# Kernel tuning notes

Hardware: AMD Instinct MI355X
Metric: run time of the kernel (lower is better)

Reference implementation:

```python
import jax, jax.numpy as jnp
import numpy as np

H = 128
B, N, E = 256, 81, 1620
LN_EPS = 1e-5


def setup_inputs() -> dict:
    key = jax.random.key(0)
    ks = jax.random.split(key, 12)
    s = 0.05
    return {
        "node_features": jax.random.normal(ks[0], (B, N, H), jnp.float32),
        "edge_index": jax.random.randint(ks[1], (2, E), 0, N, jnp.int64),
        "Wm1": jax.random.normal(ks[2], (2 * H, H), jnp.float32) * s,
        "bm1": jnp.zeros((H,), jnp.float32),
        "Wm2": jax.random.normal(ks[3], (H, H), jnp.float32) * s,
        "bm2": jnp.zeros((H,), jnp.float32),
        "Wu1": jax.random.normal(ks[4], (2 * H, H), jnp.float32) * s,
        "bu1": jnp.zeros((H,), jnp.float32),
        "Wu2": jax.random.normal(ks[5], (H, H), jnp.float32) * s,
        "bu2": jnp.zeros((H,), jnp.float32),
        "gamma": jnp.ones((H,), jnp.float32),
        "beta": jnp.zeros((H,), jnp.float32),
    }


def reference(node_features, edge_index, Wm1, bm1, Wm2, bm2, Wu1, bu1, Wu2, bu2, gamma, beta):
    src_idx, tgt_idx = edge_index[0], edge_index[1]
    # Gather: [B, E, H] each (vectorized over batch; original loops in Python)
    src = node_features[:, src_idx]
    tgt = node_features[:, tgt_idx]
    comb = jnp.concatenate([src, tgt], axis=-1)            # [B, E, 2H]
    msgs = jax.nn.relu(comb @ Wm1 + bm1) @ Wm2 + bm2       # [B, E, H]
    # Scatter-mean aggregation at target nodes
    agg = jnp.zeros_like(node_features).at[:, tgt_idx].add(msgs)  # [B, N, H]
    counts = jnp.zeros((N,), node_features.dtype).at[tgt_idx].add(1.0)
    counts = jnp.maximum(counts, 1.0)
    agg = agg / counts[None, :, None]
    # Node update MLP + residual + LayerNorm
    comb2 = jnp.concatenate([node_features, agg], axis=-1)  # [B, N, 2H]
    upd = jax.nn.relu(comb2 @ Wu1 + bu1) @ Wu2 + bu2
    x = node_features + upd
    mu = jnp.mean(x, axis=-1, keepdims=True)
    var = jnp.mean(jnp.square(x - mu), axis=-1, keepdims=True)
    return (x - mu) * jax.lax.rsqrt(var + LN_EPS) * gamma + beta
```

## Files before the change

kernel.cpp:

```cpp
#include <hip/hip_runtime.h>


#define NN 81
#define HH 128
#define EE 1620
#define NCH 12
#define CHSZ 135
#define MPAD 96
#define WB_BYTES 196608
#define OFFS_OFF (WB_BYTES)
#define CSR_OFF  (OFFS_OFF + 82 * 4)
#define BC_OFF   (CSR_OFF + EE * 4)
#define WS_NEED  (BC_OFF + HH * 4)

typedef __attribute__((ext_vector_type(8))) short bf16x8;
typedef __attribute__((ext_vector_type(8))) unsigned short ushort8v;
typedef __attribute__((ext_vector_type(4))) unsigned short ushort4v;
typedef __attribute__((ext_vector_type(4))) float f32x4;

__device__ __forceinline__ unsigned short f2b(float f) {
  union { float f; unsigned u; } v; v.f = f;
  unsigned r = v.u + 0x7fffu + ((v.u >> 16) & 1u);
  return (unsigned short)(r >> 16);
}
__device__ __forceinline__ float b2f(unsigned short h) {
  union { unsigned u; float f; } v; v.u = ((unsigned)h) << 16;
  return v.f;
}
__device__ __forceinline__ unsigned swzu(int r, int laneb) {
  return ((unsigned)(r * 256 + laneb)) ^ ((unsigned)((r & 7) << 4));
}

__global__ __launch_bounds__(1024)
void setup_kernel(const float* __restrict__ Wm1, const float* __restrict__ Wm2,
                  const float* __restrict__ Wu1, const float* __restrict__ Wu2,
                  const float* __restrict__ bm2, const int* __restrict__ eidx,
                  char* __restrict__ ws) {
  __shared__ __align__(16) char arena[81920];
  const int tid = threadIdx.x;

  if (blockIdx.x < 8) {
    const int gid = blockIdx.x * 1024 + tid;
    const int lane = gid & 63;
    const int t = gid >> 6;
    const int ks = t & 3, nt = (t >> 2) & 7, mat = t >> 5;
    const float* src;
    int slot;
    if (mat == 0)      { src = Wm1;           slot = 0; }
    else if (mat == 1) { src = Wm1 + HH * HH; slot = 1; }
    else if (mat == 2) { src = Wu1;           slot = 3; }
    else               { src = Wu2;           slot = 5; }
    const int c = nt * 16 + (lane & 15);
    const int k0 = ks * 32 + (lane >> 4) * 8;
    bf16x8 pv;
#pragma unroll
    for (int j = 0; j < 8; ++j) pv[j] = (short)f2b(src[(k0 + j) * HH + c]);
    *(bf16x8*)((unsigned short*)ws + (size_t)slot * 16384 + (((nt * 4 + ks) * 64) + lane) * 8) = pv;
    return;
  }

  if (blockIdx.x == 8) {
    int* edg   = (int*)arena;
    int* cnt   = edg + 2 * EE;
    int* tot   = cnt + NCH * NN;
    int* scanS = tot + NN;
    int* wsumS = scanS + 128;
    int* offsS = wsumS + 2;
    int* csrS  = offsS + NN + 1;
    for (int i = tid; i < 2 * EE; i += 1024) edg[i] = eidx[i];
    __syncthreads();
    if (tid < NCH * NN) {
      const int t = tid % NN, ch = tid / NN;
      const int e0 = ch * CHSZ, e1 = e0 + CHSZ;
      int c = 0;
      for (int e = e0; e < e1; ++e) c += (edg[EE + e] == t);
      cnt[ch * NN + t] = c;
    }
    __syncthreads();
    if (tid < NN) {
      int s = 0;
#pragma unroll
      for (int ch = 0; ch < NCH; ++ch) s += cnt[ch * NN + tid];
      tot[tid] = s;
    }
    __syncthreads();
    if (tid < 128) {
      const int l = tid & 63, w = tid >> 6;
      int inc = (tid < NN) ? tot[tid] : 0;
#pragma unroll
      for (int d = 1; d < 64; d <<= 1) {
        int u = __shfl_up(inc, d);
        if (l >= d) inc += u;
      }
      scanS[tid] = inc;
      if (l == 63) wsumS[w] = inc;
    }
    __syncthreads();
    if (tid < 128) {
      const int w = tid >> 6;
      const int inc = scanS[tid] + (w ? wsumS[0] : 0);
      if (tid < NN) offsS[tid] = inc - tot[tid];
      if (tid == NN - 1) offsS[NN] = inc;
    }
    __syncthreads();
    if (tid < NCH * NN) {
      const int t = tid % NN, ch = tid / NN;
      int pos = offsS[t];
      for (int c2 = 0; c2 < ch; ++c2) pos += cnt[c2 * NN + t];
      const int e0 = ch * CHSZ, e1 = e0 + CHSZ;
      for (int e = e0; e < e1; ++e)
        if (edg[EE + e] == t) csrS[pos++] = edg[e];
    }
    __syncthreads();
    int* wofs = (int*)(ws + OFFS_OFF);
    int* wcsr = (int*)(ws + CSR_OFF);
    for (int i = tid; i < NN + 1; i += 1024) wofs[i] = offsS[i];
    for (int i = tid; i < EE; i += 1024) wcsr[i] = csrS[i];
    return;
  }

  {
    const int bs = blockIdx.x - 9;
    float* WuL = (float*)arena;
    float* WmL = WuL + HH * HH;
    const float* Wu1b = Wu1 + HH * HH;
    float4* WuL4 = (float4*)WuL;
    const float4* src4 = (const float4*)Wu1b;
    for (int i = tid; i < HH * HH / 4; i += 1024) WuL4[i] = src4[i];
    const float4* wm4 = (const float4*)(Wm2 + bs * 32 * HH);
    float4* WmL4 = (float4*)WmL;
    if (tid < 32 * HH / 4) WmL4[tid] = wm4[tid];
    __syncthreads();
    const int kk = tid >> 5;
    const int k  = bs * 32 + kk;
    const int cg = tid & 31;
    f32x4 acc = (f32x4)0.f;
    for (int j = 0; j < HH; ++j) {
      const float a = WmL[kk * HH + j];
      const float4 w = WuL4[j * 32 + cg];
      acc[0] += a * w.x; acc[1] += a * w.y; acc[2] += a * w.z; acc[3] += a * w.w;
    }
    unsigned short* dst = (unsigned short*)ws;
#pragma unroll
    for (int q = 0; q < 4; ++q) {
      const int c = cg * 4 + q;
      const int nt = c >> 4;
      const int l = (((k & 31) >> 3) << 4) | (c & 15);
      dst[(size_t)2 * 16384 + (((nt * 4 + bs) * 64) + l) * 8 + (k & 7)] = f2b(acc[q]);
    }
    if (bs == 0 && tid < HH) {
      float s = 0.f;
      for (int j = 0; j < HH; ++j) s += bm2[j] * WuL[j * HH + tid];
      ((float*)(ws + BC_OFF))[tid] = s;
    }
  }
}

__device__ __forceinline__ void gemm3x1(const unsigned short* Ab, const unsigned short* Wp,
                                        int lane, int mt0, int nt0, f32x4 acc[3]) {
  bf16x8 Bf[4];
#pragma unroll
  for (int ks = 0; ks < 4; ++ks)
    Bf[ks] = *(const bf16x8*)(Wp + ((nt0 * 4 + ks) * 64 + lane) * 8);
  const int rl = lane & 15;
  const int kb = (lane >> 4) * 16;
  const unsigned swz = (unsigned)((rl & 7) << 4);
#pragma unroll
  for (int ks = 0; ks < 4; ++ks)
#pragma unroll
    for (int mm = 0; mm < 3; ++mm) {
      const int r = (mt0 + mm) * 16 + rl;
      const unsigned byte = (unsigned)(r * 256) + (((unsigned)(ks * 64 + kb)) ^ swz);
      bf16x8 a = *(const bf16x8*)((const char*)Ab + byte);
      acc[mm] = __builtin_amdgcn_mfma_f32_16x16x32_bf16(a, Bf[ks], acc[mm], 0, 0, 0);
    }
}

__device__ __forceinline__ void gemm3x1x2(const unsigned short* Ab,
                                          const unsigned short* Wp0, const unsigned short* Wp1,
                                          int lane, int mt0, int nt0,
                                          f32x4 acc0[3], f32x4 acc1[3]) {
  bf16x8 B0[4], B1[4];
#pragma unroll
  for (int ks = 0; ks < 4; ++ks) {
    B0[ks] = *(const bf16x8*)(Wp0 + ((nt0 * 4 + ks) * 64 + lane) * 8);
    B1[ks] = *(const bf16x8*)(Wp1 + ((nt0 * 4 + ks) * 64 + lane) * 8);
  }
  const int rl = lane & 15;
  const int kb = (lane >> 4) * 16;
  const unsigned swz = (unsigned)((rl & 7) << 4);
#pragma unroll
  for (int ks = 0; ks < 4; ++ks)
#pragma unroll
    for (int mm = 0; mm < 3; ++mm) {
      const int r = (mt0 + mm) * 16 + rl;
      const unsigned byte = (unsigned)(r * 256) + (((unsigned)(ks * 64 + kb)) ^ swz);
      bf16x8 a = *(const bf16x8*)((const char*)Ab + byte);
      acc0[mm] = __builtin_amdgcn_mfma_f32_16x16x32_bf16(a, B0[ks], acc0[mm], 0, 0, 0);
      acc1[mm] = __builtin_amdgcn_mfma_f32_16x16x32_bf16(a, B1[ks], acc1[mm], 0, 0, 0);
    }
}

__device__ __forceinline__ void gemm3x1_2A(const unsigned short* A0, const unsigned short* A1,
                                           const unsigned short* Wp0, const unsigned short* Wp1,
                                           int lane, int mt0, int nt0,
                                           f32x4 acc0[3], f32x4 acc1[3]) {
  bf16x8 B0[4], B1[4];
#pragma unroll
  for (int ks = 0; ks < 4; ++ks) {
    B0[ks] = *(const bf16x8*)(Wp0 + ((nt0 * 4 + ks) * 64 + lane) * 8);
    B1[ks] = *(const bf16x8*)(Wp1 + ((nt0 * 4 + ks) * 64 + lane) * 8);
  }
  const int rl = lane & 15;
  const int kb = (lane >> 4) * 16;
  const unsigned swz = (unsigned)((rl & 7) << 4);
#pragma unroll
  for (int ks = 0; ks < 4; ++ks)
#pragma unroll
    for (int mm = 0; mm < 3; ++mm) {
      const int r = (mt0 + mm) * 16 + rl;
      const unsigned byte = (unsigned)(r * 256) + (((unsigned)(ks * 64 + kb)) ^ swz);
      bf16x8 a0 = *(const bf16x8*)((const char*)A0 + byte);
      acc0[mm] = __builtin_amdgcn_mfma_f32_16x16x32_bf16(a0, B0[ks], acc0[mm], 0, 0, 0);
      bf16x8 a1 = *(const bf16x8*)((const char*)A1 + byte);
      acc1[mm] = __builtin_amdgcn_mfma_f32_16x16x32_bf16(a1, B1[ks], acc1[mm], 0, 0, 0);
    }
}

__global__ __launch_bounds__(1024, 4)
void mpnn_mfma3_kernel(const float* __restrict__ node,
                       const float* __restrict__ bm1,
                       const float* __restrict__ bu1, const float* __restrict__ bu2,
                       const float* __restrict__ gamma_, const float* __restrict__ beta_,
                       const char* __restrict__ ws,
                       float* __restrict__ out) {
  __shared__ float X[NN][HH];
  __shared__ unsigned short Xb[MPAD * HH];
  __shared__ unsigned short bufP[MPAD * HH];
  __shared__ unsigned short bufQ[MPAD * HH];
  __shared__ int   csrL[EE];
  __shared__ int   offsL[NN + 1];
  __shared__ float bias[6][HH];

  const int tid  = threadIdx.x;
  const int lane = tid & 63;
  const int wave = tid >> 6;
  const int b    = blockIdx.x;

  const unsigned short* wpk = (const unsigned short*)ws;
  const int* wofs = (const int*)(ws + OFFS_OFF);
  const int* wcsr = (const int*)(ws + CSR_OFF);
  const float* wbc = (const float*)(ws + BC_OFF);

  {
    const float4* nf4 = (const float4*)(node + (size_t)b * NN * HH);
    for (int i = tid; i < NN * HH / 4; i += 1024) {
      float4 v = nf4[i];
      const int f = i * 4, r = f >> 7, c = f & 127;
      *(float4*)&X[r][c] = v;
      ushort4v pv = { f2b(v.x), f2b(v.y), f2b(v.z), f2b(v.w) };
      *(ushort4v*)((char*)Xb + swzu(r, c * 2)) = pv;
    }
    if (tid < (MPAD - NN) * 16) {
      const int r = NN + tid / 16, m = tid % 16;
      ushort8v z = {0,0,0,0,0,0,0,0};
      *(ushort8v*)((char*)Xb + swzu(r, m * 16)) = z;
    }
    for (int i = tid; i < EE; i += 1024) csrL[i] = wcsr[i];
    if (tid < NN + 1) offsL[tid] = wofs[tid];
    if (tid < HH) {
      bias[0][tid] = bm1[tid];  bias[1][tid] = wbc[tid];
      bias[2][tid] = bu1[tid];  bias[3][tid] = bu2[tid];
      bias[4][tid] = gamma_[tid]; bias[5][tid] = beta_[tid];
    }
  }
  __syncthreads();

  const int nt0 = wave & 7;
  const int mt0 = 3 * (wave >> 3);
  const int erow = (lane >> 4) * 4;
  const int ecol = lane & 15;

  {
    f32x4 accP[3], accQ[3];
#pragma unroll
    for (int mm = 0; mm < 3; ++mm) { accP[mm] = (f32x4)0.f; accQ[mm] = (f32x4)0.f; }
    gemm3x1x2(Xb, wpk, wpk + 16384, lane, mt0, nt0, accP, accQ);
#pragma unroll
    for (int mm = 0; mm < 3; ++mm)
#pragma unroll
      for (int rg = 0; rg < 4; ++rg) {
        const int R = (mt0 + mm) * 16 + erow + rg;
        const int C = nt0 * 16 + ecol;
        const unsigned byte = swzu(R, C * 2);
        const bool ok = (R < NN);
        *(unsigned short*)((char*)bufP + byte) = ok ? f2b(accP[mm][rg]) : (unsigned short)0;
        *(unsigned short*)((char*)bufQ + byte) = ok ? f2b(accQ[mm][rg]) : (unsigned short)0;
      }
  }
  __syncthreads();

  {
    const float bm1a = bias[0][2 * lane];
    const float bm1b = bias[0][2 * lane + 1];
    const int lb = lane * 4;
    for (int t = wave; t < NN; t += 16) {
      const unsigned qbyte = swzu(t, lb);
      const unsigned pq = *(const unsigned*)((const char*)bufQ + qbyte);
      const float q0 = b2f((unsigned short)(pq & 0xffff)) + bm1a;
      const float q1 = b2f((unsigned short)(pq >> 16))    + bm1b;
      float h0 = 0.f, h1 = 0.f, g0 = 0.f, g1 = 0.f;
      int e = offsL[t];
      const int o1 = offsL[t + 1];
      for (; e + 4 <= o1; e += 4) {
        const int s0 = csrL[e], s1 = csrL[e + 1], s2 = csrL[e + 2], s3 = csrL[e + 3];
        const unsigned p0 = *(const unsigned*)((const char*)bufP + swzu(s0, lb));
        const unsigned p1 = *(const unsigned*)((const char*)bufP + swzu(s1, lb));
        const unsigned p2 = *(const unsigned*)((const char*)bufP + swzu(s2, lb));
        const unsigned p3 = *(const unsigned*)((const char*)bufP + swzu(s3, lb));
        h0 += fmaxf(b2f((unsigned short)(p0 & 0xffff)) + q0, 0.f);
        h1 += fmaxf(b2f((unsigned short)(p0 >> 16))    + q1, 0.f);
        g0 += fmaxf(b2f((unsigned short)(p1 & 0xffff)) + q0, 0.f);
        g1 += fmaxf(b2f((unsigned short)(p1 >> 16))    + q1, 0.f);
        h0 += fmaxf(b2f((unsigned short)(p2 & 0xffff)) + q0, 0.f);
        h1 += fmaxf(b2f((unsigned short)(p2 >> 16))    + q1, 0.f);
        g0 += fmaxf(b2f((unsigned short)(p3 & 0xffff)) + q0, 0.f);
        g1 += fmaxf(b2f((unsigned short)(p3 >> 16))    + q1, 0.f);
      }
      for (; e < o1; ++e) {
        const int s = csrL[e];
        const unsigned pp = *(const unsigned*)((const char*)bufP + swzu(s, lb));
        h0 += fmaxf(b2f((unsigned short)(pp & 0xffff)) + q0, 0.f);
        h1 += fmaxf(b2f((unsigned short)(pp >> 16))    + q1, 0.f);
      }
      h0 += g0; h1 += g1;
      const unsigned hv = (unsigned)f2b(h0) | ((unsigned)f2b(h1) << 16);
      *(unsigned*)((char*)bufQ + qbyte) = hv;
    }
  }
  __syncthreads();

  {
    f32x4 accT[3], accU[3];
#pragma unroll
    for (int mm = 0; mm < 3; ++mm) { accT[mm] = (f32x4)0.f; accU[mm] = (f32x4)0.f; }
    gemm3x1_2A(bufQ, Xb, wpk + 2 * 16384, wpk + 3 * 16384, lane, mt0, nt0, accT, accU);
#pragma unroll
    for (int mm = 0; mm < 3; ++mm)
#pragma unroll
      for (int rg = 0; rg < 4; ++rg) {
        const int R = (mt0 + mm) * 16 + erow + rg;
        const int C = nt0 * 16 + ecol;
        float v = 0.f;
        if (R < NN) {
          const int dg = offsL[R + 1] - offsL[R];
          const float inv = (dg > 0) ? 1.f / (float)dg : 1.f;
          const float sf  = (dg > 0) ? 1.f : 0.f;
          v = fmaxf(accU[mm][rg] + accT[mm][rg] * inv + sf * bias[1][C] + bias[2][C], 0.f);
        }
        *(unsigned short*)((char*)bufP + swzu(R, C * 2)) = f2b(v);
      }
  }
  __syncthreads();

  {
    f32x4 acc[3];
#pragma unroll
    for (int mm = 0; mm < 3; ++mm) acc[mm] = (f32x4)0.f;
    gemm3x1(bufP, wpk + 5 * 16384, lane, mt0, nt0, acc);
#pragma unroll
    for (int mm = 0; mm < 3; ++mm)
#pragma unroll
      for (int rg = 0; rg < 4; ++rg) {
        const int R = (mt0 + mm) * 16 + erow + rg;
        const int C = nt0 * 16 + ecol;
        if (R < NN) X[R][C] += acc[mm][rg] + bias[3][C];
      }
  }
  __syncthreads();

  for (int r = wave; r < NN; r += 16) {
    const float x0 = X[r][lane], x1 = X[r][lane + 64];
    float s = x0 + x1;
#pragma unroll
    for (int off = 32; off; off >>= 1) s += __shfl_xor(s, off);
    const float mu = s * (1.f / 128.f);
    const float d0 = x0 - mu, d1 = x1 - mu;
    float v = d0 * d0 + d1 * d1;
#pragma unroll
    for (int off = 32; off; off >>= 1) v += __shfl_xor(v, off);
    const float rstd = rsqrtf(v * (1.f / 128.f) + 1e-5f);
    const size_t o = ((size_t)b * NN + r) * HH;
    out[o + lane]      = d0 * rstd * bias[4][lane]      + bias[5][lane];
    out[o + lane + 64] = d1 * rstd * bias[4][lane + 64] + bias[5][lane + 64];
  }
}

__device__ __forceinline__ void gemm_acc_f32(const float (*A)[HH], const float* __restrict__ Wg,
                                             int c, int row0, int nr, float (&acc)[41]) {
  float w[8];
#pragma unroll
  for (int j = 0; j < 8; ++j) w[j] = Wg[j * HH + c];
  for (int k0 = 0; k0 < HH; k0 += 8) {
    float wn[8];
    if (k0 + 8 < HH) {
#pragma unroll
      for (int j = 0; j < 8; ++j) wn[j] = Wg[(k0 + 8 + j) * HH + c];
    }
#pragma unroll
    for (int i = 0; i < 41; ++i) {
      if (i < nr) {
        const float4 a0 = *(const float4*)&A[row0 + i][k0];
        const float4 a1 = *(const float4*)&A[row0 + i][k0 + 4];
        acc[i] += a0.x * w[0] + a0.y * w[1] + a0.z * w[2] + a0.w * w[3]
                + a1.x * w[4] + a1.y * w[5] + a1.z * w[6] + a1.w * w[7];
      }
    }
#pragma unroll
    for (int j = 0; j < 8; ++j) w[j] = wn[j];
  }
}

__global__ __launch_bounds__(256, 1)
void mpnn_fused_kernel(const float* __restrict__ node, const int* __restrict__ eidx,
                       const float* __restrict__ Wm1, const float* __restrict__ bm1,
                       const float* __restrict__ Wm2, const float* __restrict__ bm2,
                       const float* __restrict__ Wu1, const float* __restrict__ bu1,
                       const float* __restrict__ Wu2, const float* __restrict__ bu2,
                       const float* __restrict__ gamma_, const float* __restrict__ beta_,
                       float* __restrict__ out) {
  __shared__ float X[NN][HH];
  __shared__ float Pb[NN][HH];
  __shared__ float Qb[NN][HH];
  __shared__ int   edg[2 * EE];
  __shared__ int   csr[EE];
  __shared__ int   offs[NN + 1];
  __shared__ int   cnt3[3][NN];
  __shared__ int   base3[3][NN];
  __shared__ float biases[6][HH];

  const int tid  = threadIdx.x;
  const int lane = tid & 63;
  const int wave = tid >> 6;
  const int b    = blockIdx.x;

  {
    const float4* nf4 = (const float4*)(node + (size_t)b * NN * HH);
    float4* X4 = (float4*)&X[0][0];
    for (int i = tid; i < NN * HH / 4; i += 256) X4[i] = nf4[i];
    for (int i = tid; i < 2 * EE; i += 256) edg[i] = eidx[i];
    if (tid < HH) {
      biases[0][tid] = bm1[tid]; biases[1][tid] = bm2[tid];
      biases[2][tid] = bu1[tid]; biases[3][tid] = bu2[tid];
      biases[4][tid] = gamma_[tid]; biases[5][tid] = beta_[tid];
    }
  }
  __syncthreads();
  if (tid < 3 * NN) {
    const int t = tid % NN, ch = tid / NN;
    const int e0 = ch * 540, e1 = e0 + 540;
    int cnt = 0;
    for (int e = e0; e < e1; ++e) cnt += (edg[EE + e] == t);
    cnt3[ch][t] = cnt;
  }
  __syncthreads();
  if (tid == 0) {
    int run = 0;
    for (int t = 0; t < NN; ++t) {
      offs[t] = run;
      base3[0][t] = run;
      base3[1][t] = base3[0][t] + cnt3[0][t];
      base3[2][t] = base3[1][t] + cnt3[1][t];
      run = base3[2][t] + cnt3[2][t];
    }
    offs[NN] = run;
  }
  __syncthreads();
  if (tid < 3 * NN) {
    const int t = tid % NN, ch = tid / NN;
    const int e0 = ch * 540, e1 = e0 + 540;
    int pos = base3[ch][t];
    for (int e = e0; e < e1; ++e)
      if (edg[EE + e] == t) csr[pos++] = edg[e];
  }
  __syncthreads();

  const int c    = ((wave & 1) << 6) | lane;
  const int row0 = (wave >> 1) ? 41 : 0;
  const int nr   = (wave >> 1) ? 40 : 41;

  {
    float acc[41];
#pragma unroll
    for (int i = 0; i < 41; ++i) acc[i] = 0.f;
    gemm_acc_f32(X, Wm1, c, row0, nr, acc);
#pragma unroll
    for (int i = 0; i < 41; ++i) if (i < nr) Pb[row0 + i][c] = acc[i];
  }
  {
    float acc[41];
#pragma unroll
    for (int i = 0; i < 41; ++i) acc[i] = 0.f;
    gemm_acc_f32(X, Wm1 + HH * HH, c, row0, nr, acc);
#pragma unroll
    for (int i = 0; i < 41; ++i) if (i < nr) Qb[row0 + i][c] = acc[i];
  }
  __syncthreads();

  for (int t = wave; t < NN; t += 4) {
    const int o0 = offs[t], o1 = offs[t + 1];
    const float q0 = Qb[t][lane]      + biases[0][lane];
    const float q1 = Qb[t][lane + 64] + biases[0][lane + 64];
    float h0 = 0.f, h1 = 0.f;
    for (int e = o0; e < o1; ++e) {
      const int s = csr[e];
      h0 += fmaxf(Pb[s][lane]      + q0, 0.f);
      h1 += fmaxf(Pb[s][lane + 64] + q1, 0.f);
    }
    Qb[t][lane]      = h0;
    Qb[t][lane + 64] = h1;
  }
  __syncthreads();

  {
    float acc[41];
#pragma unroll
    for (int i = 0; i < 41; ++i) acc[i] = 0.f;
    gemm_acc_f32(Qb, Wm2, c, row0, nr, acc);
#pragma unroll
    for (int i = 0; i < 41; ++i) if (i < nr) {
      const int r = row0 + i;
      const float d = (float)(offs[r + 1] - offs[r]);
      Pb[r][c] = (acc[i] + d * biases[1][c]) * (1.f / fmaxf(d, 1.f));
    }
  }
  __syncthreads();

  {
    float acc[41];
#pragma unroll
    for (int i = 0; i < 41; ++i) acc[i] = 0.f;
    gemm_acc_f32(X,  Wu1,           c, row0, nr, acc);
    gemm_acc_f32(Pb, Wu1 + HH * HH, c, row0, nr, acc);
#pragma unroll
    for (int i = 0; i < 41; ++i) if (i < nr)
      Qb[row0 + i][c] = fmaxf(acc[i] + biases[2][c], 0.f);
  }
  __syncthreads();

  {
    float acc[41];
#pragma unroll
    for (int i = 0; i < 41; ++i) acc[i] = 0.f;
    gemm_acc_f32(Qb, Wu2, c, row0, nr, acc);
#pragma unroll
    for (int i = 0; i < 41; ++i) if (i < nr) {
      const int r = row0 + i;
      X[r][c] = X[r][c] + acc[i] + biases[3][c];
    }
  }
  __syncthreads();

  for (int r = wave; r < NN; r += 4) {
    const float x0 = X[r][lane], x1 = X[r][lane + 64];
    float s = x0 + x1;
#pragma unroll
    for (int off = 32; off; off >>= 1) s += __shfl_xor(s, off);
    const float mu = s * (1.f / 128.f);
    const float d0 = x0 - mu, d1 = x1 - mu;
    float v = d0 * d0 + d1 * d1;
#pragma unroll
    for (int off = 32; off; off >>= 1) v += __shfl_xor(v, off);
    const float rstd = rsqrtf(v * (1.f / 128.f) + 1e-5f);
    const size_t o = ((size_t)b * NN + r) * HH;
    out[o + lane]      = d0 * rstd * biases[4][lane]      + biases[5][lane];
    out[o + lane + 64] = d1 * rstd * biases[4][lane + 64] + biases[5][lane + 64];
  }
}

extern "C" void kernel_launch(void* const* d_in, const int* in_sizes, int n_in,
                              void* d_out, int out_size, void* d_ws, size_t ws_size,
                              hipStream_t stream) {
  (void)in_sizes; (void)n_in; (void)out_size;
  const float* node  = (const float*)d_in[0];
  const int*   eidx  = (const int*)  d_in[1];
  const float* Wm1   = (const float*)d_in[2];
  const float* bm1   = (const float*)d_in[3];
  const float* Wm2   = (const float*)d_in[4];
  const float* bm2   = (const float*)d_in[5];
  const float* Wu1   = (const float*)d_in[6];
  const float* bu1   = (const float*)d_in[7];
  const float* Wu2   = (const float*)d_in[8];
  const float* bu2   = (const float*)d_in[9];
  const float* gamma_= (const float*)d_in[10];
  const float* beta_ = (const float*)d_in[11];
  float* outp = (float*)d_out;

  if (ws_size >= (size_t)WS_NEED) {
    char* ws = (char*)d_ws;
    hipLaunchKernelGGL(setup_kernel, dim3(13), dim3(1024), 0, stream,
                       Wm1, Wm2, Wu1, Wu2, bm2, eidx, ws);
    hipLaunchKernelGGL(mpnn_mfma3_kernel, dim3(256), dim3(1024), 0, stream,
                       node, bm1, bu1, bu2, gamma_, beta_, ws, outp);
  } else {
    hipLaunchKernelGGL(mpnn_fused_kernel, dim3(256), dim3(256), 0, stream,
                       node, eidx, Wm1, bm1, Wm2, bm2, Wu1, bu1, Wu2, bu2,
                       gamma_, beta_, outp);
  }
}
```

Baseline: 45.50 us.

## Build CSR with wave ballot ranking; batch node loads and fold bias into Q

```diff
diff --git a/kernel.cpp b/kernel.cpp
--- a/kernel.cpp
+++ b/kernel.cpp
@@ -1,11 +1,11 @@
 #include <hip/hip_runtime.h>
+#include <hip/hip_bf16.h>
 
 
 #define NN 81
 #define HH 128
 #define EE 1620
-#define NCH 12
-#define CHSZ 135
+#define NCHK 26
 #define MPAD 96
 #define WB_BYTES 196608
 #define OFFS_OFF (WB_BYTES)
@@ -15,7 +15,6 @@
 
 typedef __attribute__((ext_vector_type(8))) short bf16x8;
 typedef __attribute__((ext_vector_type(8))) unsigned short ushort8v;
-typedef __attribute__((ext_vector_type(4))) unsigned short ushort4v;
 typedef __attribute__((ext_vector_type(4))) float f32x4;
 
 __device__ __forceinline__ unsigned short f2b(float f) {
@@ -26,6 +25,12 @@
 __device__ __forceinline__ float b2f(unsigned short h) {
   union { unsigned u; float f; } v; v.u = ((unsigned)h) << 16;
   return v.f;
+}
+__device__ __forceinline__ unsigned f2b2(float x, float y) {
+  float2 f; f.x = x; f.y = y;
+  union { __hip_bfloat162 h; unsigned u; } v;
+  v.h = __float22bfloat162_rn(f);
+  return v.u;
 }
 __device__ __forceinline__ unsigned swzu(int r, int laneb) {
   return ((unsigned)(r * 256 + laneb)) ^ ((unsigned)((r & 7) << 4));
@@ -60,27 +65,40 @@
   }
 
   if (blockIdx.x == 8) {
-    int* edg   = (int*)arena;
-    int* cnt   = edg + 2 * EE;
-    int* tot   = cnt + NCH * NN;
+    int* srcE  = (int*)arena;
+    int* tgtE  = srcE + EE;
+    int* rankS = tgtE + EE;
+    int* cntC  = rankS + EE;
+    int* tot   = cntC + NCHK * NN;
     int* scanS = tot + NN;
     int* wsumS = scanS + 128;
     int* offsS = wsumS + 2;
-    int* csrS  = offsS + NN + 1;
-    for (int i = tid; i < 2 * EE; i += 1024) edg[i] = eidx[i];
+    for (int i = tid; i < NCHK * NN; i += 1024) cntC[i] = 0;
+    for (int i = tid; i < 2 * EE; i += 1024) srcE[i] = eidx[i];
     __syncthreads();
-    if (tid < NCH * NN) {
-      const int t = tid % NN, ch = tid / NN;
-      const int e0 = ch * CHSZ, e1 = e0 + CHSZ;
-      int c = 0;
-      for (int e = e0; e < e1; ++e) c += (edg[EE + e] == t);
-      cnt[ch * NN + t] = c;
+    const int lane = tid & 63, wv = tid >> 6;
+    for (int c = wv; c < NCHK; c += 16) {
+      const int e = c * 64 + lane;
+      const bool ok = (e < EE);
+      const int t = ok ? tgtE[e] : -1;
+      unsigned long long mymask = 0;
+#pragma unroll
+      for (int i = 0; i < 64; ++i) {
+        const int ti = __shfl(t, i);
+        const unsigned long long bal = __ballot(t == ti);
+        if (i == lane) mymask = bal;
+      }
+      if (ok) {
+        const int rank = __popcll(mymask & ((1ull << lane) - 1ull));
+        rankS[e] = rank;
+        if (rank == 0) cntC[c * NN + t] = __popcll(mymask);
+      }
     }
     __syncthreads();
     if (tid < NN) {
       int s = 0;
 #pragma unroll
-      for (int ch = 0; ch < NCH; ++ch) s += cnt[ch * NN + tid];
+      for (int c = 0; c < NCHK; ++c) s += cntC[c * NN + tid];
       tot[tid] = s;
     }
     __syncthreads();
@@ -103,19 +121,23 @@
       if (tid == NN - 1) offsS[NN] = inc;
     }
     __syncthreads();
-    if (tid < NCH * NN) {
-      const int t = tid % NN, ch = tid / NN;
-      int pos = offsS[t];
-      for (int c2 = 0; c2 < ch; ++c2) pos += cnt[c2 * NN + t];
-      const int e0 = ch * CHSZ, e1 = e0 + CHSZ;
-      for (int e = e0; e < e1; ++e)
-        if (edg[EE + e] == t) csrS[pos++] = edg[e];
+    if (tid < NN) {
+      int run = offsS[tid];
+#pragma unroll
+      for (int c = 0; c < NCHK; ++c) {
+        const int tmp = cntC[c * NN + tid];
+        cntC[c * NN + tid] = run;
+        run += tmp;
+      }
     }
     __syncthreads();
     int* wofs = (int*)(ws + OFFS_OFF);
     int* wcsr = (int*)(ws + CSR_OFF);
-    for (int i = tid; i < NN + 1; i += 1024) wofs[i] = offsS[i];
-    for (int i = tid; i < EE; i += 1024) wcsr[i] = csrS[i];
+    for (int i = tid; i <= NN; i += 1024) wofs[i] = offsS[i];
+    for (int e = tid; e < EE; e += 1024) {
+      const int t = tgtE[e];
+      wcsr[cntC[(e >> 6) * NN + t] + rankS[e]] = srcE[e];
+    }
     return;
   }
 
@@ -228,7 +250,7 @@
 }
 
 __global__ __launch_bounds__(1024, 4)
-void mpnn_mfma3_kernel(const float* __restrict__ node,
+void mpnn_mfma4_kernel(const float* __restrict__ node,
                        const float* __restrict__ bm1,
                        const float* __restrict__ bu1, const float* __restrict__ bu2,
                        const float* __restrict__ gamma_, const float* __restrict__ beta_,
@@ -254,12 +276,21 @@
 
   {
     const float4* nf4 = (const float4*)(node + (size_t)b * NN * HH);
-    for (int i = tid; i < NN * HH / 4; i += 1024) {
-      float4 v = nf4[i];
-      const int f = i * 4, r = f >> 7, c = f & 127;
+    const int i2 = tid + 2048;
+    const bool has2 = (i2 < NN * HH / 4);
+    float4 v0 = nf4[tid];
+    float4 v1 = nf4[tid + 1024];
+    float4 v2 = has2 ? nf4[i2] : make_float4(0.f, 0.f, 0.f, 0.f);
+#pragma unroll
+    for (int k = 0; k < 3; ++k) {
+      const int i = tid + k * 1024;
+      if (k == 2 && !has2) break;
+      const float4 v = (k == 0) ? v0 : (k == 1) ? v1 : v2;
+      const int r = i >> 5, c = (i & 31) * 4;
       *(float4*)&X[r][c] = v;
-      ushort4v pv = { f2b(v.x), f2b(v.y), f2b(v.z), f2b(v.w) };
-      *(ushort4v*)((char*)Xb + swzu(r, c * 2)) = pv;
+      unsigned pk0 = f2b2(v.x, v.y), pk1 = f2b2(v.z, v.w);
+      uint2 pv; pv.x = pk0; pv.y = pk1;
+      *(uint2*)((char*)Xb + swzu(r, c * 2)) = pv;
     }
     if (tid < (MPAD - NN) * 16) {
       const int r = NN + tid / 16, m = tid % 16;
@@ -295,20 +326,18 @@
         const unsigned byte = swzu(R, C * 2);
         const bool ok = (R < NN);
         *(unsigned short*)((char*)bufP + byte) = ok ? f2b(accP[mm][rg]) : (unsigned short)0;
-        *(unsigned short*)((char*)bufQ + byte) = ok ? f2b(accQ[mm][rg]) : (unsigned short)0;
-      }
-  }
-  __syncthreads();
-
-  {
-    const float bm1a = bias[0][2 * lane];
-    const float bm1b = bias[0][2 * lane + 1];
+        *(unsigned short*)((char*)bufQ + byte) = ok ? f2b(accQ[mm][rg] + bias[0][C]) : (unsigned short)0;
+      }
+  }
+  __syncthreads();
+
+  {
     const int lb = lane * 4;
     for (int t = wave; t < NN; t += 16) {
       const unsigned qbyte = swzu(t, lb);
       const unsigned pq = *(const unsigned*)((const char*)bufQ + qbyte);
-      const float q0 = b2f((unsigned short)(pq & 0xffff)) + bm1a;
-      const float q1 = b2f((unsigned short)(pq >> 16))    + bm1b;
+      const float q0 = b2f((unsigned short)(pq & 0xffff));
+      const float q1 = b2f((unsigned short)(pq >> 16));
       float h0 = 0.f, h1 = 0.f, g0 = 0.f, g1 = 0.f;
       int e = offsL[t];
       const int o1 = offsL[t + 1];
@@ -600,7 +629,7 @@
     char* ws = (char*)d_ws;
     hipLaunchKernelGGL(setup_kernel, dim3(13), dim3(1024), 0, stream,
                        Wm1, Wm2, Wu1, Wu2, bm2, eidx, ws);
-    hipLaunchKernelGGL(mpnn_mfma3_kernel, dim3(256), dim3(1024), 0, stream,
+    hipLaunchKernelGGL(mpnn_mfma4_kernel, dim3(256), dim3(1024), 0, stream,
                        node, bm1, bu1, bu2, gamma_, beta_, ws, outp);
   } else {
     hipLaunchKernelGGL(mpnn_fused_kernel, dim3(256), dim3(256), 0, stream,
```

After: 41.78 us. 8.2% less time.
